# Kernel optimization log

Hardware: AMD Instinct MI355X
Metric: run time of the kernel (lower is better)

Reference implementation:

```python
import jax, jax.numpy as jnp
import numpy as np

N1 = 512
N2 = 512
N = N1 + N2
NEG_SLOPE = 0.2


def _build_edges(n1, n2):
    # inside: fully connected within each set, both directions
    s1, d1 = np.triu_indices(n1, 1)
    s2, d2 = np.triu_indices(n2, 1)
    is_ = np.concatenate([s1, s2 + n1])
    id_ = np.concatenate([d1, d2 + n1])
    inside = np.stack([np.concatenate([is_, id_]), np.concatenate([id_, is_])])
    # cross: fully connected bipartite, both directions
    cs = np.repeat(np.arange(n1), n2)
    cd = np.tile(np.arange(n1, n1 + n2), n1)
    cross = np.stack([np.concatenate([cs, cd]), np.concatenate([cd, cs])])
    # PyG GATConv default add_self_loops=True
    loops = np.arange(n1 + n2)
    self_e = np.stack([loops, loops])
    inside = np.concatenate([inside, self_e], axis=1)
    cross = np.concatenate([cross, self_e], axis=1)
    return inside.astype(np.int32), cross.astype(np.int32)


def setup_inputs() -> dict:
    key = jax.random.key(0)
    ks = jax.random.split(key, 12)
    inside_edge, cross_edge = _build_edges(N1, N2)
    s = 0.1
    return {
        'desc1': jax.random.normal(ks[0], (N1, 128), jnp.float32),
        'desc2': jax.random.normal(ks[1], (N2, 128), jnp.float32),
        'W1': jax.random.normal(ks[2], (128, 128), jnp.float32) * s,
        'a_src1': jax.random.normal(ks[3], (128, 1), jnp.float32) * s,
        'a_dst1': jax.random.normal(ks[4], (128, 1), jnp.float32) * s,
        'b1': jnp.zeros((128,), jnp.float32),
        'W2': jax.random.normal(ks[5], (128, 128), jnp.float32) * s,
        'a_src2': jax.random.normal(ks[6], (1, 128), jnp.float32) * s,
        'a_dst2': jax.random.normal(ks[7], (1, 128), jnp.float32) * s,
        'b2': jnp.zeros((128,), jnp.float32),
        'inside_edge': jnp.asarray(inside_edge),
        'cross_edge': jnp.asarray(cross_edge),
    }


def gat_conv(x, edge_index, W, a_src, a_dst, bias, heads, out_ch, concat):
    # x: [N, F_in]; edge_index: [2, E] (self-loops already included)
    n = x.shape[0]
    src, dst = edge_index[0], edge_index[1]
    h = (x @ W).reshape(n, heads, out_ch)                 # [N, H, C]
    a_s = jnp.sum(h * a_src, axis=-1)                     # [N, H]
    a_d = jnp.sum(h * a_dst, axis=-1)                     # [N, H]
    e = jax.nn.leaky_relu(a_s[src] + a_d[dst], NEG_SLOPE)  # [E, H]
    # segment (scatter) softmax over incoming edges of each dst node
    m = jax.ops.segment_max(e, dst, num_segments=n)
    ex = jnp.exp(e - m[dst])
    denom = jax.ops.segment_sum(ex, dst, num_segments=n)
    alpha = ex / (denom[dst] + 1e-16)                     # [E, H]
    out = jax.ops.segment_sum(alpha[:, :, None] * h[src], dst, num_segments=n)  # [N, H, C]
    out = out.reshape(n, heads * out_ch) if concat else out.mean(axis=1)
    return out + bias


def reference(desc1, desc2, W1, a_src1, a_dst1, b1, W2, a_src2, a_dst2, b2, inside_edge, cross_edge):
    x = jnp.concatenate([desc1, desc2], axis=0)  # [N, 128]
    for _ in range(2):
        x = jax.nn.elu(gat_conv(x, inside_edge, W1, a_src1, a_dst1, b1, 128, 1, True))
        x = jax.nn.elu(gat_conv(x, cross_edge, W1, a_src1, a_dst1, b1, 128, 1, True))
    x = gat_conv(x, cross_edge, W2, a_src2, a_dst2, b2, 1, 128, False)  # [N, 128]
    return x
```

## Files before the change

### kernel.cpp

```cpp
#include <hip/hip_runtime.h>
#include <hip/hip_bf16.h>


typedef __hip_bfloat16 bf16;

__device__ __forceinline__ float b2f(bf16 x) { return __bfloat162float(x); }

__device__ __forceinline__ int detect_bf16(const void* desc1) {
  const unsigned* u = (const unsigned*)desc1;
  int hits = 0;
#pragma unroll 8
  for (int i = 0; i < 256; ++i) {
    unsigned e = (u[i] >> 7) & 0xFFu;
    hits += (e >= 100u && e <= 140u) ? 1 : 0;
  }
  return hits >= 200 ? 1 : 0;
}

__device__ __forceinline__ float load_in(const void* p, int i, int bf) {
  return bf ? b2f(((const bf16*)p)[i]) : ((const float*)p)[i];
}

__global__ __launch_bounds__(256) void prep_kernel(
    const void* __restrict__ desc1, const void* __restrict__ desc2,
    const void* __restrict__ W1,   const void* __restrict__ as1,
    const void* __restrict__ ad1,  const void* __restrict__ b1,
    const void* __restrict__ W2,   const void* __restrict__ as2,
    const void* __restrict__ ad2,  const void* __restrict__ b2,
    float* __restrict__ xt, float* __restrict__ W1f, float* __restrict__ W2f,
    float* __restrict__ vecs, int* __restrict__ flag) {
  const int bf = detect_bf16(desc1);
  if (blockIdx.x == 0 && threadIdx.x == 0) *flag = bf;
  const int total = 131072 + 16384 + 16384 + 6 * 128;
  for (int idx = blockIdx.x * blockDim.x + threadIdx.x; idx < total;
       idx += gridDim.x * blockDim.x) {
    if (idx < 131072) {
      int n = idx & 1023, c = idx >> 10;
      float v = (n < 512) ? load_in(desc1, n * 128 + c, bf)
                          : load_in(desc2, (n - 512) * 128 + c, bf);
      xt[((c >> 2) * 1024 + n) * 4 + (c & 3)] = v;
    } else if (idx < 147456) {
      W1f[idx - 131072] = load_in(W1, idx - 131072, bf);
    } else if (idx < 163840) {
      W2f[idx - 147456] = load_in(W2, idx - 147456, bf);
    } else {
      int i = idx - 163840, o = i & 127;
      float v;
      if      (i < 128) v = load_in(as1, o, bf);
      else if (i < 256) v = load_in(ad1, o, bf);
      else if (i < 384) v = load_in(b1, o, bf);
      else if (i < 512) v = load_in(as2, o, bf);
      else if (i < 640) v = load_in(ad2, o, bf);
      else              v = load_in(b2, o, bf);
      vecs[i] = v;
    }
  }
}

template <int CROSS>
__global__ __launch_bounds__(512, 2) void layer_kernel(
    const float* __restrict__ xt_in, float* __restrict__ xt_out,
    const float* __restrict__ Wf, const float* __restrict__ vecs) {
  __shared__ float    sS[512];
  __shared__ float    sH[512];
  __shared__ unsigned hA[512];
  __shared__ unsigned ISb[512];
  __shared__ unsigned binNext[512];
  __shared__ float2   PRE[512];
  __shared__ float2   SUF[512];
  __shared__ float    red[16];
  __shared__ unsigned wTot[8];
  __shared__ float2   preTot[8];
  __shared__ float2   sufTot[8];

  const int tid  = threadIdx.x;
  const int lane = tid & 63;
  const int wave = tid >> 6;
  const int hd   = blockIdx.x & 127;
  const int S    = blockIdx.x >> 7;
  const int D    = CROSS ? (1 - S) : S;
  const float a_src = vecs[hd], a_dst = vecs[128 + hd], bias = vecs[256 + hd];

  float accS0 = 0.f, accS1 = 0.f, accD0 = 0.f, accD1 = 0.f;
  {
    const float4* x4 = (const float4*)xt_in;
    const int nS = S * 512 + tid;
    const int nD = D * 512 + tid;
    for (int cc = 0; cc < 32; cc += 8) {
      float4 xs[8], xd[8];
#pragma unroll
      for (int u = 0; u < 8; ++u) {
        xs[u] = x4[(cc + u) * 1024 + nS];
        if (CROSS) xd[u] = x4[(cc + u) * 1024 + nD];
      }
#pragma unroll
      for (int u = 0; u < 8; ++u) {
        const int k = (cc + u) * 4;
        const float w0 = Wf[k * 128 + hd];
        const float w1 = Wf[(k + 1) * 128 + hd];
        const float w2 = Wf[(k + 2) * 128 + hd];
        const float w3 = Wf[(k + 3) * 128 + hd];
        accS0 = fmaf(xs[u].x, w0, accS0);
        accS1 = fmaf(xs[u].y, w1, accS1);
        accS0 = fmaf(xs[u].z, w2, accS0);
        accS1 = fmaf(xs[u].w, w3, accS1);
        if (CROSS) {
          accD0 = fmaf(xd[u].x, w0, accD0);
          accD1 = fmaf(xd[u].y, w1, accD1);
          accD0 = fmaf(xd[u].z, w2, accD0);
          accD1 = fmaf(xd[u].w, w3, accD1);
        }
      }
    }
  }
  const float h_src = accS0 + accS1;
  const float h_dst = CROSS ? (accD0 + accD1) : h_src;
  const float s_own = h_src * a_src;
  const float d_own = h_dst * a_dst;

  {
    float mnw = s_own, mxw = s_own;
#pragma unroll
    for (int off = 32; off > 0; off >>= 1) {
      mnw = fminf(mnw, __shfl_down(mnw, off));
      mxw = fmaxf(mxw, __shfl_down(mxw, off));
    }
    if (lane == 0) { red[wave] = mnw; red[8 + wave] = mxw; }
  }
  hA[tid] = 0;
  binNext[tid] = 0;
  __syncthreads();
  const float mn = fminf(fminf(fminf(red[0], red[1]), fminf(red[2], red[3])),
                         fminf(fminf(red[4], red[5]), fminf(red[6], red[7])));
  const float mx = fmaxf(fmaxf(fmaxf(red[8], red[9]), fmaxf(red[10], red[11])),
                         fmaxf(fmaxf(red[12], red[13]), fmaxf(red[14], red[15])));
  const float scale = 512.0f / fmaxf(mx - mn, 1e-20f);

  const int myBin = (int)fminf(fmaxf((s_own - mn) * scale, 0.0f), 511.0f);
  atomicAdd(&hA[myBin], 1u);
  __syncthreads();

  {
    unsigned v = hA[tid];
#pragma unroll
    for (int off = 1; off < 64; off <<= 1) {
      unsigned u = __shfl_up(v, off);
      if (lane >= off) v += u;
    }
    if (lane == 63) wTot[wave] = v;
    __syncthreads();
    unsigned pre = 0;
#pragma unroll
    for (int w = 0; w < 8; ++w) pre += (w < wave) ? wTot[w] : 0u;
    ISb[tid] = v + pre;
    __syncthreads();
  }

  {
    unsigned base = myBin ? ISb[myBin - 1] : 0u;
    unsigned pos = base + atomicAdd(&binNext[myBin], 1u);
    sS[pos] = s_own;
    sH[pos] = h_src;
  }
  __syncthreads();

  {
    const float sv = sS[tid];
    const float hv = sH[tid];
    const float e1 = __expf(sv), e2 = __expf(0.2f * sv);
    float p0 = e2, p1 = e2 * hv;
    float q0 = e1, q1 = e1 * hv;
#pragma unroll
    for (int off = 1; off < 64; off <<= 1) {
      float u0 = __shfl_up(p0, off), u1 = __shfl_up(p1, off);
      if (lane >= off) { p0 += u0; p1 += u1; }
      float v0 = __shfl_down(q0, off), v1 = __shfl_down(q1, off);
      if (lane + off < 64) { q0 += v0; q1 += v1; }
    }
    if (lane == 63) preTot[wave] = make_float2(p0, p1);
    if (lane == 0)  sufTot[wave] = make_float2(q0, q1);
    __syncthreads();
    float a0 = 0.f, a1 = 0.f, b0 = 0.f, b1 = 0.f;
#pragma unroll
    for (int w = 0; w < 8; ++w) {
      float2 pt = preTot[w], st = sufTot[w];
      if (w < wave) { a0 += pt.x; a1 += pt.y; }
      if (w > wave) { b0 += st.x; b1 += st.y; }
    }
    PRE[tid] = make_float2(p0 + a0, p1 + a1);
    SUF[tid] = make_float2(q0 + b0, q1 + b1);
    __syncthreads();
  }

  {
    const float theta = -d_own;
    int b = (int)fminf(fmaxf((theta - mn) * scale, 0.0f), 511.0f);
    unsigned k0 = b ? ISb[b - 1] : 0u;
    unsigned k1 = ISb[b];
    float F1 = __expf(d_own), F2 = __expf(0.2f * d_own);
    float P2 = 0.f, P2h = 0.f, S1 = 0.f, S1h = 0.f;
    if (k0 > 0)   { float2 t2 = PRE[k0 - 1]; P2 = t2.x; P2h = t2.y; }
    if (k1 < 512) { float2 t2 = SUF[k1];     S1 = t2.x; S1h = t2.y; }
    float den = F1 * S1 + F2 * P2;
    float num = F1 * S1h + F2 * P2h;
    for (unsigned e = k0; e < k1; ++e) {
      float se = sS[e], he = sH[e];
      float p = (se >= theta) ? F1 * __expf(se) : F2 * __expf(0.2f * se);
      den += p;
      num = fmaf(p, he, num);
    }
    if (CROSS) {
      float t = h_dst * a_src + d_own;
      float p = __expf(fmaxf(t, 0.2f * t));
      den += p;
      num = fmaf(p, h_dst, num);
    }
    float o = num / (den + 1e-16f) + bias;
    o = (o > 0.f) ? o : expm1f(o);
    xt_out[(((hd >> 2) * 1024) + D * 512 + tid) * 4 + (hd & 3)] = o;
  }
}

__global__ __launch_bounds__(256, 2) void mm2_kernel(
    const float* __restrict__ xt_in, const float* __restrict__ W2f,
    const float* __restrict__ vecs, float* __restrict__ h2,
    float* __restrict__ s2, float* __restrict__ d2) {
  __shared__ float rs[256], rd[256];
  const int tid = threadIdx.x;
  const int row = blockIdx.x * 2 + (tid >> 7);
  const int c = tid & 127;
  float acc0 = 0.f, acc1 = 0.f;
  {
    const float4* x4 = (const float4*)xt_in;
    for (int cc = 0; cc < 32; cc += 8) {
      float4 xb[8];
#pragma unroll
      for (int u = 0; u < 8; ++u) xb[u] = x4[(cc + u) * 1024 + row];
#pragma unroll
      for (int u = 0; u < 8; ++u) {
        const int k = (cc + u) * 4;
        acc0 = fmaf(xb[u].x, W2f[k * 128 + c],       acc0);
        acc1 = fmaf(xb[u].y, W2f[(k + 1) * 128 + c], acc1);
        acc0 = fmaf(xb[u].z, W2f[(k + 2) * 128 + c], acc0);
        acc1 = fmaf(xb[u].w, W2f[(k + 3) * 128 + c], acc1);
      }
    }
  }
  float acc = acc0 + acc1;
  h2[row * 128 + c] = acc;
  rs[tid] = acc * vecs[384 + c];
  rd[tid] = acc * vecs[512 + c];
  __syncthreads();
  for (int off = 64; off > 0; off >>= 1) {
    if ((tid & 127) < off) { rs[tid] += rs[tid + off]; rd[tid] += rd[tid + off]; }
    __syncthreads();
  }
  if ((tid & 127) == 0) {
    s2[row] = rs[tid];
    d2[row] = rd[tid];
  }
}

__global__ __launch_bounds__(256, 1) void att2_kernel(
    const float* __restrict__ h2, const float* __restrict__ s2,
    const float* __restrict__ d2, const float* __restrict__ vecs,
    void* __restrict__ out, const int* __restrict__ flag) {
  __shared__ __align__(16) float pT[512 * 4];
  const int tid = threadIdx.x;
  const int dstBase = blockIdx.x * 4;
  const int srcBase = (dstBase < 512) ? 512 : 0;

  for (int e = tid; e < 2048; e += 256) {
    int j = e >> 2, ld = e & 3;
    float t = s2[srcBase + j] + d2[dstBase + ld];
    pT[e] = __expf(fmaxf(t, 0.2f * t));
  }
  __syncthreads();

  const int c = tid & 127;
  const int g = tid >> 7;
  const int i0 = dstBase + 2 * g, i1 = i0 + 1;
  float den0 = 0.f, num0 = 0.f, den1 = 0.f, num1 = 0.f;
  const float* hrow = h2 + srcBase * 128 + c;
  for (int j0 = 0; j0 < 512; j0 += 8) {
    float hb[8];
#pragma unroll
    for (int u = 0; u < 8; ++u) hb[u] = hrow[(j0 + u) * 128];
#pragma unroll
    for (int u = 0; u < 8; ++u) {
      float2 pv = *(const float2*)(pT + (j0 + u) * 4 + 2 * g);
      den0 += pv.x; num0 = fmaf(pv.x, hb[u], num0);
      den1 += pv.y; num1 = fmaf(pv.y, hb[u], num1);
    }
  }
  float ts0 = s2[i0] + d2[i0];
  float ps0 = __expf(fmaxf(ts0, 0.2f * ts0));
  den0 += ps0; num0 = fmaf(ps0, h2[i0 * 128 + c], num0);
  float ts1 = s2[i1] + d2[i1];
  float ps1 = __expf(fmaxf(ts1, 0.2f * ts1));
  den1 += ps1; num1 = fmaf(ps1, h2[i1 * 128 + c], num1);

  float o0 = num0 / (den0 + 1e-16f) + vecs[640 + c];
  float o1 = num1 / (den1 + 1e-16f) + vecs[640 + c];
  if (*flag) {
    ((bf16*)out)[i0 * 128 + c] = __float2bfloat16(o0);
    ((bf16*)out)[i1 * 128 + c] = __float2bfloat16(o1);
  } else {
    ((float*)out)[i0 * 128 + c] = o0;
    ((float*)out)[i1 * 128 + c] = o1;
  }
}

extern "C" void kernel_launch(void* const* d_in, const int* in_sizes, int n_in,
                              void* d_out, int out_size, void* d_ws, size_t ws_size,
                              hipStream_t stream) {
  (void)in_sizes; (void)n_in; (void)out_size; (void)ws_size;
  float* ws   = (float*)d_ws;
  float* xtA  = ws;
  float* xtB  = ws + 131072;
  float* h2   = ws + 262144;
  float* W1f  = ws + 393216;
  float* W2f  = ws + 409600;
  float* vecs = ws + 425984;
  float* s2   = ws + 426752;
  float* d2   = ws + 427776;
  int*   flag = (int*)(ws + 428800);

  prep_kernel<<<64, 256, 0, stream>>>(d_in[0], d_in[1], d_in[2], d_in[3],
                                      d_in[4], d_in[5], d_in[6], d_in[7],
                                      d_in[8], d_in[9], xtA, W1f, W2f, vecs, flag);
  layer_kernel<0><<<256, 512, 0, stream>>>(xtA, xtB, W1f, vecs);
  layer_kernel<1><<<256, 512, 0, stream>>>(xtB, xtA, W1f, vecs);
  layer_kernel<0><<<256, 512, 0, stream>>>(xtA, xtB, W1f, vecs);
  layer_kernel<1><<<256, 512, 0, stream>>>(xtB, xtA, W1f, vecs);
  mm2_kernel<<<512, 256, 0, stream>>>(xtA, W2f, vecs, h2, s2, d2);
  att2_kernel<<<256, 256, 0, stream>>>(h2, s2, d2, vecs, d_out, flag);
}
```

Measured before the change: 168.7 us.

## Fuse layer, mm2 and attention kernels into one persistent kernel with grid barriers

Replaces six separate kernel launches with one persistent 256-block kernel. Phases are separated by a software grid-wide barrier built on atomic counters in workspace, and the mm2 and att2 phases are remapped to 512 threads per block. This removes launch gaps and per-kernel ramp-up and drain. It relies on all 256 blocks being co-resident, which risks deadlock otherwise, and adds barrier spin costs.

```diff
diff --git a/kernel.cpp b/kernel.cpp
--- a/kernel.cpp
+++ b/kernel.cpp
@@ -28,9 +28,14 @@
     const void* __restrict__ W2,   const void* __restrict__ as2,
     const void* __restrict__ ad2,  const void* __restrict__ b2,
     float* __restrict__ xt, float* __restrict__ W1f, float* __restrict__ W2f,
-    float* __restrict__ vecs, int* __restrict__ flag) {
+    float* __restrict__ vecs, int* __restrict__ flag,
+    unsigned* __restrict__ bar) {
   const int bf = detect_bf16(desc1);
-  if (blockIdx.x == 0 && threadIdx.x == 0) *flag = bf;
+  if (blockIdx.x == 0 && threadIdx.x == 0) {
+    *flag = bf;
+    bar[0] = 0u;
+    bar[1] = 0u;
+  }
   const int total = 131072 + 16384 + 16384 + 6 * 128;
   for (int idx = blockIdx.x * blockDim.x + threadIdx.x; idx < total;
        idx += gridDim.x * blockDim.x) {
@@ -57,21 +62,44 @@
   }
 }
 
+__device__ __forceinline__ void grid_sync(unsigned* bar) {
+  __syncthreads();
+  if (threadIdx.x == 0) {
+    __threadfence();
+    unsigned g = __hip_atomic_load(&bar[1], __ATOMIC_RELAXED,
+                                   __HIP_MEMORY_SCOPE_AGENT);
+    unsigned a = __hip_atomic_fetch_add(&bar[0], 1u, __ATOMIC_ACQ_REL,
+                                        __HIP_MEMORY_SCOPE_AGENT);
+    if (a == gridDim.x - 1) {
+      __hip_atomic_store(&bar[0], 0u, __ATOMIC_RELAXED,
+                         __HIP_MEMORY_SCOPE_AGENT);
+      __hip_atomic_fetch_add(&bar[1], 1u, __ATOMIC_RELEASE,
+                             __HIP_MEMORY_SCOPE_AGENT);
+    } else {
+      while (__hip_atomic_load(&bar[1], __ATOMIC_ACQUIRE,
+                               __HIP_MEMORY_SCOPE_AGENT) == g)
+        __builtin_amdgcn_s_sleep(1);
+    }
+    __threadfence();
+  }
+  __syncthreads();
+}
+
 template <int CROSS>
-__global__ __launch_bounds__(512, 2) void layer_kernel(
-    const float* __restrict__ xt_in, float* __restrict__ xt_out,
+__device__ __forceinline__ void layer_phase(
+    char* smem, const float* __restrict__ xt_in, float* __restrict__ xt_out,
     const float* __restrict__ Wf, const float* __restrict__ vecs) {
-  __shared__ float    sS[512];
-  __shared__ float    sH[512];
-  __shared__ unsigned hA[512];
-  __shared__ unsigned ISb[512];
-  __shared__ unsigned binNext[512];
-  __shared__ float2   PRE[512];
-  __shared__ float2   SUF[512];
-  __shared__ float    red[16];
-  __shared__ unsigned wTot[8];
-  __shared__ float2   preTot[8];
-  __shared__ float2   sufTot[8];
+  float*    sS      = (float*)(smem);
+  float*    sH      = (float*)(smem + 2048);
+  unsigned* hA      = (unsigned*)(smem + 4096);
+  unsigned* ISb     = (unsigned*)(smem + 6144);
+  unsigned* binNext = (unsigned*)(smem + 8192);
+  float2*   PRE     = (float2*)(smem + 10240);
+  float2*   SUF     = (float2*)(smem + 14336);
+  float*    red     = (float*)(smem + 18432);
+  unsigned* wTot    = (unsigned*)(smem + 18496);
+  float2*   preTot  = (float2*)(smem + 18528);
+  float2*   sufTot  = (float2*)(smem + 18592);
 
   const int tid  = threadIdx.x;
   const int lane = tid & 63;
@@ -221,13 +249,14 @@
   }
 }
 
-__global__ __launch_bounds__(256, 2) void mm2_kernel(
-    const float* __restrict__ xt_in, const float* __restrict__ W2f,
+__device__ __forceinline__ void mm2_phase(
+    char* smem, const float* __restrict__ xt_in, const float* __restrict__ W2f,
     const float* __restrict__ vecs, float* __restrict__ h2,
     float* __restrict__ s2, float* __restrict__ d2) {
-  __shared__ float rs[256], rd[256];
+  float* rs = (float*)(smem);
+  float* rd = (float*)(smem + 2048);
   const int tid = threadIdx.x;
-  const int row = blockIdx.x * 2 + (tid >> 7);
+  const int row = blockIdx.x * 4 + (tid >> 7);
   const int c = tid & 127;
   float acc0 = 0.f, acc1 = 0.f;
   {
@@ -261,16 +290,16 @@
   }
 }
 
-__global__ __launch_bounds__(256, 1) void att2_kernel(
-    const float* __restrict__ h2, const float* __restrict__ s2,
+__device__ __forceinline__ void att2_phase(
+    char* smem, const float* __restrict__ h2, const float* __restrict__ s2,
     const float* __restrict__ d2, const float* __restrict__ vecs,
-    void* __restrict__ out, const int* __restrict__ flag) {
-  __shared__ __align__(16) float pT[512 * 4];
+    void* __restrict__ out, int bf) {
+  float* pT = (float*)smem;
   const int tid = threadIdx.x;
   const int dstBase = blockIdx.x * 4;
   const int srcBase = (dstBase < 512) ? 512 : 0;
 
-  for (int e = tid; e < 2048; e += 256) {
+  for (int e = tid; e < 2048; e += 512) {
     int j = e >> 2, ld = e & 3;
     float t = s2[srcBase + j] + d2[dstBase + ld];
     pT[e] = __expf(fmaxf(t, 0.2f * t));
@@ -279,8 +308,8 @@
 
   const int c = tid & 127;
   const int g = tid >> 7;
-  const int i0 = dstBase + 2 * g, i1 = i0 + 1;
-  float den0 = 0.f, num0 = 0.f, den1 = 0.f, num1 = 0.f;
+  const int i0 = dstBase + g;
+  float den = 0.f, num = 0.f;
   const float* hrow = h2 + srcBase * 128 + c;
   for (int j0 = 0; j0 < 512; j0 += 8) {
     float hb[8];
@@ -288,27 +317,41 @@
     for (int u = 0; u < 8; ++u) hb[u] = hrow[(j0 + u) * 128];
 #pragma unroll
     for (int u = 0; u < 8; ++u) {
-      float2 pv = *(const float2*)(pT + (j0 + u) * 4 + 2 * g);
-      den0 += pv.x; num0 = fmaf(pv.x, hb[u], num0);
-      den1 += pv.y; num1 = fmaf(pv.y, hb[u], num1);
-    }
-  }
-  float ts0 = s2[i0] + d2[i0];
-  float ps0 = __expf(fmaxf(ts0, 0.2f * ts0));
-  den0 += ps0; num0 = fmaf(ps0, h2[i0 * 128 + c], num0);
-  float ts1 = s2[i1] + d2[i1];
-  float ps1 = __expf(fmaxf(ts1, 0.2f * ts1));
-  den1 += ps1; num1 = fmaf(ps1, h2[i1 * 128 + c], num1);
-
-  float o0 = num0 / (den0 + 1e-16f) + vecs[640 + c];
-  float o1 = num1 / (den1 + 1e-16f) + vecs[640 + c];
-  if (*flag) {
-    ((bf16*)out)[i0 * 128 + c] = __float2bfloat16(o0);
-    ((bf16*)out)[i1 * 128 + c] = __float2bfloat16(o1);
-  } else {
-    ((float*)out)[i0 * 128 + c] = o0;
-    ((float*)out)[i1 * 128 + c] = o1;
-  }
+      float p = pT[(j0 + u) * 4 + g];
+      den += p;
+      num = fmaf(p, hb[u], num);
+    }
+  }
+  float ts = s2[i0] + d2[i0];
+  float ps = __expf(fmaxf(ts, 0.2f * ts));
+  den += ps;
+  num = fmaf(ps, h2[i0 * 128 + c], num);
+
+  float o = num / (den + 1e-16f) + vecs[640 + c];
+  if (bf) ((bf16*)out)[i0 * 128 + c] = __float2bfloat16(o);
+  else    ((float*)out)[i0 * 128 + c] = o;
+}
+
+__global__ __launch_bounds__(512, 2) void fused_kernel(
+    float* __restrict__ xtA, float* __restrict__ xtB,
+    const float* __restrict__ W1f, const float* __restrict__ W2f,
+    const float* __restrict__ vecs, float* __restrict__ h2,
+    float* __restrict__ s2, float* __restrict__ d2,
+    void* __restrict__ out, const int* __restrict__ flag,
+    unsigned* __restrict__ bar) {
+  __shared__ __align__(16) char smem[18944];
+
+  layer_phase<0>(smem, xtA, xtB, W1f, vecs);
+  grid_sync(bar);
+  layer_phase<1>(smem, xtB, xtA, W1f, vecs);
+  grid_sync(bar);
+  layer_phase<0>(smem, xtA, xtB, W1f, vecs);
+  grid_sync(bar);
+  layer_phase<1>(smem, xtB, xtA, W1f, vecs);
+  grid_sync(bar);
+  mm2_phase(smem, xtA, W2f, vecs, h2, s2, d2);
+  grid_sync(bar);
+  att2_phase(smem, h2, s2, d2, vecs, out, *flag);
 }
 
 extern "C" void kernel_launch(void* const* d_in, const int* in_sizes, int n_in,
@@ -325,14 +368,12 @@
   float* s2   = ws + 426752;
   float* d2   = ws + 427776;
   int*   flag = (int*)(ws + 428800);
+  unsigned* bar = (unsigned*)(ws + 428804);
 
   prep_kernel<<<64, 256, 0, stream>>>(d_in[0], d_in[1], d_in[2], d_in[3],
                                       d_in[4], d_in[5], d_in[6], d_in[7],
-                                      d_in[8], d_in[9], xtA, W1f, W2f, vecs, flag);
-  layer_kernel<0><<<256, 512, 0, stream>>>(xtA, xtB, W1f, vecs);
-  layer_kernel<1><<<256, 512, 0, stream>>>(xtB, xtA, W1f, vecs);
-  layer_kernel<0><<<256, 512, 0, stream>>>(xtA, xtB, W1f, vecs);
-  layer_kernel<1><<<256, 512, 0, stream>>>(xtB, xtA, W1f, vecs);
-  mm2_kernel<<<512, 256, 0, stream>>>(xtA, W2f, vecs, h2, s2, d2);
-  att2_kernel<<<256, 256, 0, stream>>>(h2, s2, d2, vecs, d_out, flag);
-}
+                                      d_in[8], d_in[9], xtA, W1f, W2f, vecs,
+                                      flag, bar);
+  fused_kernel<<<256, 512, 0, stream>>>(xtA, xtB, W1f, W2f, vecs, h2, s2, d2,
+                                        d_out, flag, bar);
+}
```

Result: slower. 343.0 us (+103.3%).

## Split GEMM out of fused GAT layer kernel and halve att2 work per block

Applied to the files above, without the earlier changes.

Moves the x@W1 projection out of each attention layer kernel into a separate gemm kernel that writes H transposed to workspace. In the old kernel each block recomputed a column, and cross layers computed it twice. The weight column is now staged in shared memory from a transposed W1 copy. att2 now processes 2 destination nodes per block over 512 blocks instead of 4 over 256, and prep launches more blocks. The cost is four extra launches and a round trip of H through global memory.

```diff
diff --git a/kernel.cpp b/kernel.cpp
--- a/kernel.cpp
+++ b/kernel.cpp
@@ -27,7 +27,7 @@
     const void* __restrict__ ad1,  const void* __restrict__ b1,
     const void* __restrict__ W2,   const void* __restrict__ as2,
     const void* __restrict__ ad2,  const void* __restrict__ b2,
-    float* __restrict__ xt, float* __restrict__ W1f, float* __restrict__ W2f,
+    float* __restrict__ xt, float* __restrict__ W1t, float* __restrict__ W2f,
     float* __restrict__ vecs, int* __restrict__ flag) {
   const int bf = detect_bf16(desc1);
   if (blockIdx.x == 0 && threadIdx.x == 0) *flag = bf;
@@ -40,7 +40,8 @@
                           : load_in(desc2, (n - 512) * 128 + c, bf);
       xt[((c >> 2) * 1024 + n) * 4 + (c & 3)] = v;
     } else if (idx < 147456) {
-      W1f[idx - 131072] = load_in(W1, idx - 131072, bf);
+      int i = idx - 131072, hd = i >> 7, k = i & 127;
+      W1t[i] = load_in(W1, k * 128 + hd, bf);
     } else if (idx < 163840) {
       W2f[idx - 147456] = load_in(W2, idx - 147456, bf);
     } else {
@@ -57,10 +58,38 @@
   }
 }
 
+__global__ __launch_bounds__(256, 2) void gemm_kernel(
+    const float* __restrict__ xt_in, const float* __restrict__ W1t,
+    float* __restrict__ Ht) {
+  __shared__ float wcol[128];
+  const int tid = threadIdx.x;
+  const int hd = blockIdx.x & 127;
+  const int chunk = blockIdx.x >> 7;
+  const int node = chunk * 256 + tid;
+  if (tid < 32) ((float4*)wcol)[tid] = ((const float4*)(W1t + hd * 128))[tid];
+  __syncthreads();
+  const float4* x4 = (const float4*)xt_in;
+  float acc0 = 0.f, acc1 = 0.f;
+  for (int cc = 0; cc < 32; cc += 8) {
+    float4 xs[8];
+#pragma unroll
+    for (int u = 0; u < 8; ++u) xs[u] = x4[(cc + u) * 1024 + node];
+#pragma unroll
+    for (int u = 0; u < 8; ++u) {
+      const int k = (cc + u) * 4;
+      acc0 = fmaf(xs[u].x, wcol[k],     acc0);
+      acc1 = fmaf(xs[u].y, wcol[k + 1], acc1);
+      acc0 = fmaf(xs[u].z, wcol[k + 2], acc0);
+      acc1 = fmaf(xs[u].w, wcol[k + 3], acc1);
+    }
+  }
+  Ht[hd * 1024 + node] = acc0 + acc1;
+}
+
 template <int CROSS>
-__global__ __launch_bounds__(512, 2) void layer_kernel(
-    const float* __restrict__ xt_in, float* __restrict__ xt_out,
-    const float* __restrict__ Wf, const float* __restrict__ vecs) {
+__global__ __launch_bounds__(512, 2) void attn_kernel(
+    const float* __restrict__ Ht, float* __restrict__ xt_out,
+    const float* __restrict__ vecs) {
   __shared__ float    sS[512];
   __shared__ float    sH[512];
   __shared__ unsigned hA[512];
@@ -81,40 +110,8 @@
   const int D    = CROSS ? (1 - S) : S;
   const float a_src = vecs[hd], a_dst = vecs[128 + hd], bias = vecs[256 + hd];
 
-  float accS0 = 0.f, accS1 = 0.f, accD0 = 0.f, accD1 = 0.f;
-  {
-    const float4* x4 = (const float4*)xt_in;
-    const int nS = S * 512 + tid;
-    const int nD = D * 512 + tid;
-    for (int cc = 0; cc < 32; cc += 8) {
-      float4 xs[8], xd[8];
-#pragma unroll
-      for (int u = 0; u < 8; ++u) {
-        xs[u] = x4[(cc + u) * 1024 + nS];
-        if (CROSS) xd[u] = x4[(cc + u) * 1024 + nD];
-      }
-#pragma unroll
-      for (int u = 0; u < 8; ++u) {
-        const int k = (cc + u) * 4;
-        const float w0 = Wf[k * 128 + hd];
-        const float w1 = Wf[(k + 1) * 128 + hd];
-        const float w2 = Wf[(k + 2) * 128 + hd];
-        const float w3 = Wf[(k + 3) * 128 + hd];
-        accS0 = fmaf(xs[u].x, w0, accS0);
-        accS1 = fmaf(xs[u].y, w1, accS1);
-        accS0 = fmaf(xs[u].z, w2, accS0);
-        accS1 = fmaf(xs[u].w, w3, accS1);
-        if (CROSS) {
-          accD0 = fmaf(xd[u].x, w0, accD0);
-          accD1 = fmaf(xd[u].y, w1, accD1);
-          accD0 = fmaf(xd[u].z, w2, accD0);
-          accD1 = fmaf(xd[u].w, w3, accD1);
-        }
-      }
-    }
-  }
-  const float h_src = accS0 + accS1;
-  const float h_dst = CROSS ? (accD0 + accD1) : h_src;
+  const float h_src = Ht[hd * 1024 + S * 512 + tid];
+  const float h_dst = CROSS ? Ht[hd * 1024 + D * 512 + tid] : h_src;
   const float s_own = h_src * a_src;
   const float d_own = h_dst * a_dst;
 
@@ -261,17 +258,17 @@
   }
 }
 
-__global__ __launch_bounds__(256, 1) void att2_kernel(
+__global__ __launch_bounds__(256, 2) void att2_kernel(
     const float* __restrict__ h2, const float* __restrict__ s2,
     const float* __restrict__ d2, const float* __restrict__ vecs,
     void* __restrict__ out, const int* __restrict__ flag) {
-  __shared__ __align__(16) float pT[512 * 4];
+  __shared__ __align__(16) float pT[512 * 2];
   const int tid = threadIdx.x;
-  const int dstBase = blockIdx.x * 4;
+  const int dstBase = blockIdx.x * 2;
   const int srcBase = (dstBase < 512) ? 512 : 0;
 
-  for (int e = tid; e < 2048; e += 256) {
-    int j = e >> 2, ld = e & 3;
+  for (int e = tid; e < 1024; e += 256) {
+    int j = e >> 1, ld = e & 1;
     float t = s2[srcBase + j] + d2[dstBase + ld];
     pT[e] = __expf(fmaxf(t, 0.2f * t));
   }
@@ -279,8 +276,8 @@
 
   const int c = tid & 127;
   const int g = tid >> 7;
-  const int i0 = dstBase + 2 * g, i1 = i0 + 1;
-  float den0 = 0.f, num0 = 0.f, den1 = 0.f, num1 = 0.f;
+  const int i0 = dstBase + g;
+  float den = 0.f, num = 0.f;
   const float* hrow = h2 + srcBase * 128 + c;
   for (int j0 = 0; j0 < 512; j0 += 8) {
     float hb[8];
@@ -288,27 +285,19 @@
     for (int u = 0; u < 8; ++u) hb[u] = hrow[(j0 + u) * 128];
 #pragma unroll
     for (int u = 0; u < 8; ++u) {
-      float2 pv = *(const float2*)(pT + (j0 + u) * 4 + 2 * g);
-      den0 += pv.x; num0 = fmaf(pv.x, hb[u], num0);
-      den1 += pv.y; num1 = fmaf(pv.y, hb[u], num1);
-    }
-  }
-  float ts0 = s2[i0] + d2[i0];
-  float ps0 = __expf(fmaxf(ts0, 0.2f * ts0));
-  den0 += ps0; num0 = fmaf(ps0, h2[i0 * 128 + c], num0);
-  float ts1 = s2[i1] + d2[i1];
-  float ps1 = __expf(fmaxf(ts1, 0.2f * ts1));
-  den1 += ps1; num1 = fmaf(ps1, h2[i1 * 128 + c], num1);
-
-  float o0 = num0 / (den0 + 1e-16f) + vecs[640 + c];
-  float o1 = num1 / (den1 + 1e-16f) + vecs[640 + c];
-  if (*flag) {
-    ((bf16*)out)[i0 * 128 + c] = __float2bfloat16(o0);
-    ((bf16*)out)[i1 * 128 + c] = __float2bfloat16(o1);
-  } else {
-    ((float*)out)[i0 * 128 + c] = o0;
-    ((float*)out)[i1 * 128 + c] = o1;
-  }
+      float p = pT[(j0 + u) * 2 + g];
+      den += p;
+      num = fmaf(p, hb[u], num);
+    }
+  }
+  float ts = s2[i0] + d2[i0];
+  float ps = __expf(fmaxf(ts, 0.2f * ts));
+  den += ps;
+  num = fmaf(ps, h2[i0 * 128 + c], num);
+
+  float o = num / (den + 1e-16f) + vecs[640 + c];
+  if (*flag) ((bf16*)out)[i0 * 128 + c] = __float2bfloat16(o);
+  else       ((float*)out)[i0 * 128 + c] = o;
 }
 
 extern "C" void kernel_launch(void* const* d_in, const int* in_sizes, int n_in,
@@ -319,20 +308,26 @@
   float* xtA  = ws;
   float* xtB  = ws + 131072;
   float* h2   = ws + 262144;
-  float* W1f  = ws + 393216;
+  float* Ht   = h2;
+  float* W1t  = ws + 393216;
   float* W2f  = ws + 409600;
   float* vecs = ws + 425984;
   float* s2   = ws + 426752;
   float* d2   = ws + 427776;
   int*   flag = (int*)(ws + 428800);
 
-  prep_kernel<<<64, 256, 0, stream>>>(d_in[0], d_in[1], d_in[2], d_in[3],
-                                      d_in[4], d_in[5], d_in[6], d_in[7],
-                                      d_in[8], d_in[9], xtA, W1f, W2f, vecs, flag);
-  layer_kernel<0><<<256, 512, 0, stream>>>(xtA, xtB, W1f, vecs);
-  layer_kernel<1><<<256, 512, 0, stream>>>(xtB, xtA, W1f, vecs);
-  layer_kernel<0><<<256, 512, 0, stream>>>(xtA, xtB, W1f, vecs);
-  layer_kernel<1><<<256, 512, 0, stream>>>(xtB, xtA, W1f, vecs);
+  prep_kernel<<<128, 256, 0, stream>>>(d_in[0], d_in[1], d_in[2], d_in[3],
+                                       d_in[4], d_in[5], d_in[6], d_in[7],
+                                       d_in[8], d_in[9], xtA, W1t, W2f, vecs,
+                                       flag);
+  gemm_kernel<<<512, 256, 0, stream>>>(xtA, W1t, Ht);
+  attn_kernel<0><<<256, 512, 0, stream>>>(Ht, xtB, vecs);
+  gemm_kernel<<<512, 256, 0, stream>>>(xtB, W1t, Ht);
+  attn_kernel<1><<<256, 512, 0, stream>>>(Ht, xtA, vecs);
+  gemm_kernel<<<512, 256, 0, stream>>>(xtA, W1t, Ht);
+  attn_kernel<0><<<256, 512, 0, stream>>>(Ht, xtB, vecs);
+  gemm_kernel<<<512, 256, 0, stream>>>(xtB, W1t, Ht);
+  attn_kernel<1><<<256, 512, 0, stream>>>(Ht, xtA, vecs);
   mm2_kernel<<<512, 256, 0, stream>>>(xtA, W2f, vecs, h2, s2, d2);
-  att2_kernel<<<256, 256, 0, stream>>>(h2, s2, d2, vecs, d_out, flag);
-}
+  att2_kernel<<<512, 256, 0, stream>>>(h2, s2, d2, vecs, d_out, flag);
+}
```

Result: no change. 166.2 us (-1.5%).
